# Kernel tuning notes

Measured on AMD Instinct MI355X. Metric: run time of the kernel, lower is better.

Reference implementation:

```python
import jax, jax.numpy as jnp
import numpy as np

LAYERS = 3       # opt.layer
B = 4096         # batch of sessions
MAX_LEN = 200    # padded session length
N_ITEMS = 100000 # item vocab (index 0 is PAD after zero-row concat)
E = 112          # emb_size (SessConv default)
EPS = 1e-12      # F.normalize eps


def setup_inputs() -> dict:
    key = jax.random.key(0)
    k0, k1, k2, k3, k4 = jax.random.split(key, 5)
    item_embedding = jax.random.normal(k0, (N_ITEMS, E), dtype=jnp.float32) * 0.1
    # Session-session adjacency A and diagonal inverse-degree D (so D @ A is row-normalized)
    A = jax.random.uniform(k1, (B, B), dtype=jnp.float32)
    D = jnp.diag(1.0 / A.sum(axis=1))
    # Padded session item indices; 0 == PAD row (zeros prepended to the table)
    session_item = jax.random.randint(k2, (B, MAX_LEN), 0, N_ITEMS + 1, dtype=jnp.int64)
    session_len = jax.random.randint(k3, (B, 1), 1, MAX_LEN + 1).astype(jnp.float32)
    # layers x Linear(E, E, bias=False) weights, torch layout [out, in]
    Ws = jax.random.normal(k4, (LAYERS, E, E), dtype=jnp.float32) * (1.0 / np.sqrt(E))
    return {"item_embedding": item_embedding, "D": D, "A": A,
            "session_len": session_len, "Ws": Ws, "session_item": session_item}


def reference(item_embedding, D, A, session_len, Ws, session_item):
    # Prepend zero row so index 0 gathers zeros (padding)
    emb = jnp.concatenate([jnp.zeros((1, E), item_embedding.dtype), item_embedding], axis=0)
    # Fused ragged gather + mean-pool (replaces per-session index_select + cpu/numpy roundtrip)
    seq_h = emb[session_item]                       # [B, MAX_LEN, E]
    session_emb = seq_h.sum(axis=1) / session_len   # [B, E]
    DA = D @ A                                      # [B, B]
    acc = session_emb                               # layer-0 term of the final average
    for i in range(LAYERS):
        session_emb = session_emb @ Ws[i].T         # Linear(E,E,bias=False)
        session_emb = DA @ session_emb              # session graph propagation
        nrm = jnp.linalg.norm(session_emb, axis=-1, keepdims=True)
        acc = acc + session_emb / jnp.maximum(nrm, EPS)  # appended term is L2-normalized
        # NOTE: next layer consumes the UN-normalized session_emb (as in the torch code)
    return acc / (LAYERS + 1)
```

## Files before the change

kernel.cpp:

```cpp
#include <hip/hip_runtime.h>
#include <hip/hip_bf16.h>

#define BSZ 4096
#define MAXLEN 200
#define EDIM 112
#define NKC 16

typedef __attribute__((ext_vector_type(8))) short bf16x8;
typedef __attribute__((ext_vector_type(4))) float f32x4;

static __device__ __forceinline__ short f2bf(float f) {
    unsigned u = __float_as_uint(f);
    unsigned r = (u + 0x7fffu + ((u >> 16) & 1u)) >> 16;
    return (short)r;
}
static __device__ __forceinline__ float bf2f(short s) {
    return __uint_as_float(((unsigned)(unsigned short)s) << 16);
}
static __device__ __forceinline__ bf16x8 cvt8(float4 a, float4 b) {
    bf16x8 r;
    r[0] = f2bf(a.x); r[1] = f2bf(a.y); r[2] = f2bf(a.z); r[3] = f2bf(a.w);
    r[4] = f2bf(b.x); r[5] = f2bf(b.y); r[6] = f2bf(b.z); r[7] = f2bf(b.w);
    return r;
}
static __device__ __forceinline__ unsigned pack2(float a, float b) {
    return ((unsigned)f2bf(a) & 0xffffu) | ((unsigned)f2bf(b) << 16);
}

__global__ __launch_bounds__(256) void f32_to_bf16(const float* __restrict__ src,
                                                   unsigned short* __restrict__ dst,
                                                   int ngroups, int zgroups) {
    int g = blockIdx.x * 256 + threadIdx.x;
    if (g >= ngroups) return;
    bf16x8 o;
    if (g < zgroups) {
        #pragma unroll
        for (int i = 0; i < 8; ++i) o[i] = 0;
    } else {
        const float* p = src + (size_t)(g - zgroups) * 8;
        float4 a = *(const float4*)p;
        float4 b = *(const float4*)(p + 4);
        o = cvt8(a, b);
    }
    *(bf16x8*)(dst + (size_t)g * 8) = o;
}

__global__ __launch_bounds__(256) void gather_pool_bf(const unsigned short* __restrict__ Ebf,
                                                      const int* __restrict__ items,
                                                      const float* __restrict__ slen,
                                                      float* __restrict__ S,
                                                      float* __restrict__ acc) {
    __shared__ float part[16][14][8];
    int wave = threadIdx.x >> 6;
    int lane = threadIdx.x & 63;
    int b = blockIdx.x;
    int rg = lane / 14;
    int c  = lane % 14;
    const int* it = items + (size_t)b * MAXLEN + wave * 50;
    float a[8];
    #pragma unroll
    for (int e = 0; e < 8; ++e) a[e] = 0.f;
    if (lane < 56) {
        #pragma unroll
        for (int t = 0; t < 13; ++t) {
            int j = t * 4 + rg;
            int idx = 0;
            if (j < 50) idx = it[j];
            bf16x8 v = *(const bf16x8*)(Ebf + (size_t)idx * EDIM + c * 8);
            #pragma unroll
            for (int e = 0; e < 8; ++e) a[e] += bf2f(v[e]);
        }
        #pragma unroll
        for (int e = 0; e < 8; ++e) part[wave * 4 + rg][c][e] = a[e];
    }
    __syncthreads();
    int tid = threadIdx.x;
    if (tid < EDIM) {
        int cc = tid >> 3, ee = tid & 7;
        float s = 0.f;
        #pragma unroll
        for (int g = 0; g < 16; ++g) s += part[g][cc][ee];
        s /= slen[b];
        S[(size_t)b * EDIM + tid]   = s;
        acc[(size_t)b * EDIM + tid] = s;
    }
}

static __device__ __forceinline__ bf16x8 ldcvt(const float* p, bool valid) {
    if (valid) {
        float4 a = *(const float4*)p;
        float4 b = *(const float4*)(p + 4);
        return cvt8(a, b);
    }
    bf16x8 z;
    #pragma unroll
    for (int i = 0; i < 8; ++i) z[i] = 0;
    return z;
}

template <int MODE>
__global__ __launch_bounds__(64, 4) void fused_mid(const float* __restrict__ Sin,
                                                   const float* __restrict__ Yp,
                                                   const float* __restrict__ Dm,
                                                   float* __restrict__ accb,
                                                   const float* __restrict__ W,
                                                   unsigned short* __restrict__ Bsw) {
    __shared__ unsigned short Ylds[16][136];
    int lane = threadIdx.x;
    int gw = blockIdx.x;
    int j0 = gw * 16;
    int nrow = lane & 15;
    int quad = lane >> 4;
    int ses = j0 + nrow;

    float4 v[7];
    if (MODE == 0) {
        const float4* p = (const float4*)(Sin + (size_t)ses * EDIM + quad * 28);
        #pragma unroll
        for (int i = 0; i < 7; ++i) v[i] = p[i];
    } else {
        #pragma unroll
        for (int i = 0; i < 7; ++i) v[i] = make_float4(0.f, 0.f, 0.f, 0.f);
        #pragma unroll 4
        for (int pp = 0; pp < NKC; ++pp) {
            const float4* p = (const float4*)(Yp + (size_t)pp * BSZ * EDIM
                                              + (size_t)ses * EDIM + quad * 28);
            #pragma unroll
            for (int i = 0; i < 7; ++i) {
                float4 t = p[i];
                v[i].x += t.x; v[i].y += t.y; v[i].z += t.z; v[i].w += t.w;
            }
        }
        float d = Dm[(size_t)ses * (BSZ + 1)];
        float ss = 0.f;
        #pragma unroll
        for (int i = 0; i < 7; ++i) {
            v[i].x *= d; v[i].y *= d; v[i].z *= d; v[i].w *= d;
            ss += v[i].x * v[i].x + v[i].y * v[i].y + v[i].z * v[i].z + v[i].w * v[i].w;
        }
        ss += __shfl_xor(ss, 16, 64);
        ss += __shfl_xor(ss, 32, 64);
        float rinv = 1.f / fmaxf(sqrtf(ss), 1e-12f);
        float4* pa = (float4*)(accb + (size_t)ses * EDIM + quad * 28);
        #pragma unroll
        for (int i = 0; i < 7; ++i) {
            float4 a = pa[i];
            a.x += v[i].x * rinv; a.y += v[i].y * rinv;
            a.z += v[i].z * rinv; a.w += v[i].w * rinv;
            pa[i] = a;
        }
    }

    #pragma unroll
    for (int i = 0; i < 7; ++i) {
        uint2 pk;
        pk.x = pack2(v[i].x, v[i].y);
        pk.y = pack2(v[i].z, v[i].w);
        *(uint2*)&Ylds[nrow][quad * 28 + i * 4] = pk;
    }
    *(uint2*)&Ylds[nrow][112 + quad * 4] = make_uint2(0u, 0u);
    __syncthreads();

    bf16x8 aF[4];
    #pragma unroll
    for (int k32 = 0; k32 < 4; ++k32)
        aF[k32] = *(bf16x8*)&Ylds[nrow][k32 * 32 + quad * 8];

    f32x4 acc[7];
    #pragma unroll
    for (int t = 0; t < 7; ++t) acc[t] = (f32x4){0.f, 0.f, 0.f, 0.f};
    #pragma unroll
    for (int t = 0; t < 7; ++t) {
        const float* wr = W + (size_t)(16 * t + nrow) * EDIM;
        #pragma unroll
        for (int k32 = 0; k32 < 4; ++k32) {
            bf16x8 bF = ldcvt(wr + k32 * 32 + quad * 8, (k32 < 3) || (quad < 2));
            acc[t] = __builtin_amdgcn_mfma_f32_16x16x32_bf16(aF[k32], bF, acc[t], 0, 0, 0);
        }
    }

    int k32f = j0 >> 5;
    int qp = ((j0 >> 4) & 1) * 2 + (quad >> 1);
    int e0 = (quad & 1) * 4;
    #pragma unroll
    for (int t = 0; t < 7; ++t) {
        uint2 pk;
        pk.x = pack2(acc[t][0], acc[t][1]);
        pk.y = pack2(acc[t][2], acc[t][3]);
        *(uint2*)(Bsw + ((size_t)(k32f * 7 + t) * 64 + qp * 16 + nrow) * 8 + e0) = pk;
    }
}

template <int AMODE>
__global__ __launch_bounds__(64, 4) void big_gemm(const float* __restrict__ Af,
                                                  unsigned short* __restrict__ Asw,
                                                  const unsigned short* __restrict__ Bsw,
                                                  float* __restrict__ Yp) {
    int lane = threadIdx.x;
    int mt2 = blockIdx.x & 127;
    int kc = blockIdx.x >> 7;
    int nrow = lane & 15;
    int quad = lane >> 4;

    f32x4 acc[2][7];
    #pragma unroll
    for (int s = 0; s < 2; ++s)
        #pragma unroll
        for (int t = 0; t < 7; ++t) acc[s][t] = (f32x4){0.f, 0.f, 0.f, 0.f};

    for (int ks = 0; ks < 8; ++ks) {
        int k32 = kc * 8 + ks;
        bf16x8 aF[2];
        #pragma unroll
        for (int sub = 0; sub < 2; ++sub) {
            int mtile = mt2 * 2 + sub;
            size_t afrag = ((size_t)(mtile * 128 + k32) * 64 + lane) * 8;
            if (AMODE == 0) {
                const float* p = Af + (size_t)(mtile * 16 + nrow) * 4096 + k32 * 32 + quad * 8;
                float4 a0 = *(const float4*)p;
                float4 a1 = *(const float4*)(p + 4);
                aF[sub] = cvt8(a0, a1);
                *(bf16x8*)(Asw + afrag) = aF[sub];
            } else {
                aF[sub] = *(const bf16x8*)(Asw + afrag);
            }
        }
        const unsigned short* bb = Bsw + ((size_t)k32 * 7 * 64 + lane) * 8;
        #pragma unroll
        for (int t = 0; t < 7; ++t) {
            bf16x8 bF = *(const bf16x8*)(bb + (size_t)t * 512);
            acc[0][t] = __builtin_amdgcn_mfma_f32_16x16x32_bf16(aF[0], bF, acc[0][t], 0, 0, 0);
            acc[1][t] = __builtin_amdgcn_mfma_f32_16x16x32_bf16(aF[1], bF, acc[1][t], 0, 0, 0);
        }
    }

    float* dst = Yp + (size_t)kc * BSZ * EDIM + (size_t)mt2 * 32 * EDIM;
    #pragma unroll
    for (int sub = 0; sub < 2; ++sub)
        #pragma unroll
        for (int t = 0; t < 7; ++t)
            #pragma unroll
            for (int r = 0; r < 4; ++r)
                dst[(size_t)(sub * 16 + quad * 4 + r) * EDIM + 16 * t + nrow] = acc[sub][t][r];
}

__global__ __launch_bounds__(256) void final_epilogue(const float* __restrict__ Yp,
                                                      const float* __restrict__ Dm,
                                                      const float* __restrict__ accb,
                                                      float* __restrict__ out) {
    int wave = threadIdx.x >> 6;
    int lane = threadIdx.x & 63;
    int b = blockIdx.x * 4 + wave;

    float2 v = make_float2(0.f, 0.f);
    size_t o2 = (size_t)b * 56 + lane;
    if (lane < 56) {
        #pragma unroll 4
        for (int p = 0; p < NKC; ++p) {
            float2 t = ((const float2*)(Yp + (size_t)p * BSZ * EDIM))[o2];
            v.x += t.x;
            v.y += t.y;
        }
    }
    float d = Dm[(size_t)b * (BSZ + 1)];
    v.x *= d; v.y *= d;
    float ss = v.x * v.x + v.y * v.y;
    #pragma unroll
    for (int off = 32; off; off >>= 1) ss += __shfl_xor(ss, off, 64);
    float nrm = fmaxf(sqrtf(ss), 1e-12f);
    if (lane < 56) {
        float2 a = ((const float2*)accb)[o2];
        ((float2*)out)[o2] = make_float2((a.x + v.x / nrm) * 0.25f,
                                         (a.y + v.y / nrm) * 0.25f);
    }
}

extern "C" void kernel_launch(void* const* d_in, const int* in_sizes, int n_in,
                              void* d_out, int out_size, void* d_ws, size_t ws_size,
                              hipStream_t stream) {
    (void)in_sizes; (void)n_in; (void)out_size; (void)ws_size;
    const float* emb   = (const float*)d_in[0];
    const float* Dm    = (const float*)d_in[1];
    const float* A     = (const float*)d_in[2];
    const float* slen  = (const float*)d_in[3];
    const float* Ws    = (const float*)d_in[4];
    const int*   items = (const int*)d_in[5];
    float* out = (float*)d_out;

    char* w = (char*)d_ws;
    float* Sa   = (float*)w;
    float* accb = Sa + BSZ * EDIM;
    float* Yp   = accb + BSZ * EDIM;
    unsigned short* Bsw = (unsigned short*)(Yp + (size_t)NKC * BSZ * EDIM);
    unsigned short* Ebf = Bsw + 128 * 7 * 64 * 8;
    unsigned short* Asw = Ebf + 100001 * EDIM;

    f32_to_bf16<<<5470, 256, 0, stream>>>(emb, Ebf, 1400014, 14);
    gather_pool_bf<<<BSZ, 256, 0, stream>>>(Ebf, items, slen, Sa, accb);
    fused_mid<0><<<256, 64, 0, stream>>>(Sa, nullptr, nullptr, nullptr, Ws, Bsw);
    big_gemm<0><<<2048, 64, 0, stream>>>(A, Asw, Bsw, Yp);
    fused_mid<1><<<256, 64, 0, stream>>>(nullptr, Yp, Dm, accb,
                                         Ws + (size_t)EDIM * EDIM, Bsw);
    big_gemm<1><<<2048, 64, 0, stream>>>(nullptr, Asw, Bsw, Yp);
    fused_mid<1><<<256, 64, 0, stream>>>(nullptr, Yp, Dm, accb,
                                         Ws + (size_t)2 * EDIM * EDIM, Bsw);
    big_gemm<1><<<2048, 64, 0, stream>>>(nullptr, Asw, Bsw, Yp);
    final_epilogue<<<BSZ / 4, 256, 0, stream>>>(Yp, Dm, accb, out);
}
```

Measured before the change: 288.9 us.

## Fuse split-K reduction, normalize and next-layer linear into big GEMM blocks

Each big GEMM block now covers one 16-row M tile with 8 waves splitting K across the whole 4096 dimension. It reduces the partial sums in LDS instead of writing 16 split-K partials to global memory. The D scaling, L2 normalization, accumulator update and the next layer's 112x112 linear are done in the same kernel, with ping-pong B buffers, which removes the separate mid and final epilogue kernels and the Yp round-trip. The K loop is also software-pipelined with register prefetch. The trade-off is only 256 blocks of 512 threads and heavy LDS use, which may underfill the GPU.

```diff
diff --git a/kernel.cpp b/kernel.cpp
--- a/kernel.cpp
+++ b/kernel.cpp
@@ -4,7 +4,7 @@
 #define BSZ 4096
 #define MAXLEN 200
 #define EDIM 112
-#define NKC 16
+#define NW 8
 
 typedef __attribute__((ext_vector_type(8))) short bf16x8;
 typedef __attribute__((ext_vector_type(4))) float f32x4;
@@ -88,7 +88,7 @@
 
 static __device__ __forceinline__ bf16x8 ldcvt(const float* p, bool valid) {
     if (valid) {
-        float4 a = *(const float4*)p;
+        float4 a = *(const float4*)(p);
         float4 b = *(const float4*)(p + 4);
         return cvt8(a, b);
     }
@@ -98,13 +98,9 @@
     return z;
 }
 
-template <int MODE>
-__global__ __launch_bounds__(64, 4) void fused_mid(const float* __restrict__ Sin,
-                                                   const float* __restrict__ Yp,
-                                                   const float* __restrict__ Dm,
-                                                   float* __restrict__ accb,
-                                                   const float* __restrict__ W,
-                                                   unsigned short* __restrict__ Bsw) {
+__global__ __launch_bounds__(64, 4) void fused_mid0(const float* __restrict__ Sin,
+                                                    const float* __restrict__ W,
+                                                    unsigned short* __restrict__ Bsw) {
     __shared__ unsigned short Ylds[16][136];
     int lane = threadIdx.x;
     int gw = blockIdx.x;
@@ -114,42 +110,9 @@
     int ses = j0 + nrow;
 
     float4 v[7];
-    if (MODE == 0) {
-        const float4* p = (const float4*)(Sin + (size_t)ses * EDIM + quad * 28);
-        #pragma unroll
-        for (int i = 0; i < 7; ++i) v[i] = p[i];
-    } else {
-        #pragma unroll
-        for (int i = 0; i < 7; ++i) v[i] = make_float4(0.f, 0.f, 0.f, 0.f);
-        #pragma unroll 4
-        for (int pp = 0; pp < NKC; ++pp) {
-            const float4* p = (const float4*)(Yp + (size_t)pp * BSZ * EDIM
-                                              + (size_t)ses * EDIM + quad * 28);
-            #pragma unroll
-            for (int i = 0; i < 7; ++i) {
-                float4 t = p[i];
-                v[i].x += t.x; v[i].y += t.y; v[i].z += t.z; v[i].w += t.w;
-            }
-        }
-        float d = Dm[(size_t)ses * (BSZ + 1)];
-        float ss = 0.f;
-        #pragma unroll
-        for (int i = 0; i < 7; ++i) {
-            v[i].x *= d; v[i].y *= d; v[i].z *= d; v[i].w *= d;
-            ss += v[i].x * v[i].x + v[i].y * v[i].y + v[i].z * v[i].z + v[i].w * v[i].w;
-        }
-        ss += __shfl_xor(ss, 16, 64);
-        ss += __shfl_xor(ss, 32, 64);
-        float rinv = 1.f / fmaxf(sqrtf(ss), 1e-12f);
-        float4* pa = (float4*)(accb + (size_t)ses * EDIM + quad * 28);
-        #pragma unroll
-        for (int i = 0; i < 7; ++i) {
-            float4 a = pa[i];
-            a.x += v[i].x * rinv; a.y += v[i].y * rinv;
-            a.z += v[i].z * rinv; a.w += v[i].w * rinv;
-            pa[i] = a;
-        }
-    }
+    const float4* p = (const float4*)(Sin + (size_t)ses * EDIM + quad * 28);
+    #pragma unroll
+    for (int i = 0; i < 7; ++i) v[i] = p[i];
 
     #pragma unroll
     for (int i = 0; i < 7; ++i) {
@@ -191,87 +154,145 @@
     }
 }
 
-template <int AMODE>
-__global__ __launch_bounds__(64, 4) void big_gemm(const float* __restrict__ Af,
-                                                  unsigned short* __restrict__ Asw,
-                                                  const unsigned short* __restrict__ Bsw,
-                                                  float* __restrict__ Yp) {
-    int lane = threadIdx.x;
-    int mt2 = blockIdx.x & 127;
-    int kc = blockIdx.x >> 7;
+template <int AMODE, int LAST>
+__global__ __launch_bounds__(512, 2) void bg_fused(const float* __restrict__ Af,
+                                                   unsigned short* __restrict__ Asw,
+                                                   const unsigned short* __restrict__ Bsw,
+                                                   const float* __restrict__ Dm,
+                                                   float* __restrict__ accb,
+                                                   const float* __restrict__ W,
+                                                   unsigned short* __restrict__ BswOut,
+                                                   float* __restrict__ out) {
+    __shared__ float part[NW][16][116];
+    __shared__ unsigned short Ylds[16][136];
+    int tid = threadIdx.x;
+    int w = tid >> 6;
+    int lane = tid & 63;
     int nrow = lane & 15;
     int quad = lane >> 4;
-
-    f32x4 acc[2][7];
-    #pragma unroll
-    for (int s = 0; s < 2; ++s)
-        #pragma unroll
-        for (int t = 0; t < 7; ++t) acc[s][t] = (f32x4){0.f, 0.f, 0.f, 0.f};
-
-    for (int ks = 0; ks < 8; ++ks) {
-        int k32 = kc * 8 + ks;
-        bf16x8 aF[2];
-        #pragma unroll
-        for (int sub = 0; sub < 2; ++sub) {
-            int mtile = mt2 * 2 + sub;
-            size_t afrag = ((size_t)(mtile * 128 + k32) * 64 + lane) * 8;
-            if (AMODE == 0) {
-                const float* p = Af + (size_t)(mtile * 16 + nrow) * 4096 + k32 * 32 + quad * 8;
-                float4 a0 = *(const float4*)p;
-                float4 a1 = *(const float4*)(p + 4);
-                aF[sub] = cvt8(a0, a1);
-                *(bf16x8*)(Asw + afrag) = aF[sub];
-            } else {
-                aF[sub] = *(const bf16x8*)(Asw + afrag);
+    int mtile = blockIdx.x;
+
+    f32x4 acc[7];
+    #pragma unroll
+    for (int t = 0; t < 7; ++t) acc[t] = (f32x4){0.f, 0.f, 0.f, 0.f};
+
+    auto LOADA = [&](int k32) -> bf16x8 {
+        size_t afrag = ((size_t)(mtile * 128 + k32) * 64 + lane) * 8;
+        if (AMODE == 0) {
+            const float* p = Af + (size_t)(mtile * 16 + nrow) * 4096 + k32 * 32 + quad * 8;
+            float4 a0 = *(const float4*)p;
+            float4 a1 = *(const float4*)(p + 4);
+            bf16x8 r = cvt8(a0, a1);
+            *(bf16x8*)(Asw + afrag) = r;
+            return r;
+        } else {
+            return *(const bf16x8*)(Asw + afrag);
+        }
+    };
+
+    int k32 = w * 16;
+    bf16x8 aF = LOADA(k32);
+    bf16x8 bF[7];
+    {
+        const unsigned short* bb = Bsw + ((size_t)k32 * 7 * 64 + lane) * 8;
+        #pragma unroll
+        for (int t = 0; t < 7; ++t) bF[t] = *(const bf16x8*)(bb + (size_t)t * 512);
+    }
+    #pragma unroll 1
+    for (int ks = 0; ks < 15; ++ks) {
+        bf16x8 aN = LOADA(k32 + 1);
+        bf16x8 bN[7];
+        const unsigned short* bb = Bsw + ((size_t)(k32 + 1) * 7 * 64 + lane) * 8;
+        #pragma unroll
+        for (int t = 0; t < 7; ++t) bN[t] = *(const bf16x8*)(bb + (size_t)t * 512);
+        #pragma unroll
+        for (int t = 0; t < 7; ++t)
+            acc[t] = __builtin_amdgcn_mfma_f32_16x16x32_bf16(aF, bF[t], acc[t], 0, 0, 0);
+        aF = aN;
+        #pragma unroll
+        for (int t = 0; t < 7; ++t) bF[t] = bN[t];
+        ++k32;
+    }
+    #pragma unroll
+    for (int t = 0; t < 7; ++t)
+        acc[t] = __builtin_amdgcn_mfma_f32_16x16x32_bf16(aF, bF[t], acc[t], 0, 0, 0);
+
+    #pragma unroll
+    for (int t = 0; t < 7; ++t)
+        #pragma unroll
+        for (int r = 0; r < 4; ++r)
+            part[w][quad * 4 + r][16 * t + nrow] = acc[t][r];
+    __syncthreads();
+
+    int half = lane >> 5;
+    int cg = lane & 31;
+    int row = 2 * w + half;
+    int grow = mtile * 16 + row;
+    int col = cg * 4;
+    float4 v = make_float4(0.f, 0.f, 0.f, 0.f);
+    if (cg < 28) {
+        #pragma unroll
+        for (int p = 0; p < NW; ++p) {
+            float4 t = *(const float4*)&part[p][row][col];
+            v.x += t.x; v.y += t.y; v.z += t.z; v.w += t.w;
+        }
+    }
+    float d = Dm[(size_t)grow * (BSZ + 1)];
+    v.x *= d; v.y *= d; v.z *= d; v.w *= d;
+    float ss = v.x * v.x + v.y * v.y + v.z * v.z + v.w * v.w;
+    ss += __shfl_xor(ss, 1, 64);
+    ss += __shfl_xor(ss, 2, 64);
+    ss += __shfl_xor(ss, 4, 64);
+    ss += __shfl_xor(ss, 8, 64);
+    ss += __shfl_xor(ss, 16, 64);
+    float rinv = 1.f / fmaxf(sqrtf(ss), 1e-12f);
+    if (cg < 28) {
+        if (LAST) {
+            float4 a = *(const float4*)(accb + (size_t)grow * EDIM + col);
+            float4 o;
+            o.x = (a.x + v.x * rinv) * 0.25f;
+            o.y = (a.y + v.y * rinv) * 0.25f;
+            o.z = (a.z + v.z * rinv) * 0.25f;
+            o.w = (a.w + v.w * rinv) * 0.25f;
+            *(float4*)(out + (size_t)grow * EDIM + col) = o;
+        } else {
+            float4* pa = (float4*)(accb + (size_t)grow * EDIM + col);
+            float4 a = *pa;
+            a.x += v.x * rinv; a.y += v.y * rinv;
+            a.z += v.z * rinv; a.w += v.w * rinv;
+            *pa = a;
+        }
+    }
+
+    if (!LAST) {
+        uint2 pk;
+        pk.x = pack2(v.x, v.y);
+        pk.y = pack2(v.z, v.w);
+        *(uint2*)&Ylds[row][col] = pk;
+        __syncthreads();
+
+        if (w < 7) {
+            int t = w;
+            bf16x8 aF2[4];
+            #pragma unroll
+            for (int k = 0; k < 4; ++k)
+                aF2[k] = *(bf16x8*)&Ylds[nrow][k * 32 + quad * 8];
+            f32x4 c = (f32x4){0.f, 0.f, 0.f, 0.f};
+            const float* wr = W + (size_t)(16 * t + nrow) * EDIM;
+            #pragma unroll
+            for (int k = 0; k < 4; ++k) {
+                bf16x8 bW = ldcvt(wr + k * 32 + quad * 8, (k < 3) || (quad < 2));
+                c = __builtin_amdgcn_mfma_f32_16x16x32_bf16(aF2[k], bW, c, 0, 0, 0);
             }
-        }
-        const unsigned short* bb = Bsw + ((size_t)k32 * 7 * 64 + lane) * 8;
-        #pragma unroll
-        for (int t = 0; t < 7; ++t) {
-            bf16x8 bF = *(const bf16x8*)(bb + (size_t)t * 512);
-            acc[0][t] = __builtin_amdgcn_mfma_f32_16x16x32_bf16(aF[0], bF, acc[0][t], 0, 0, 0);
-            acc[1][t] = __builtin_amdgcn_mfma_f32_16x16x32_bf16(aF[1], bF, acc[1][t], 0, 0, 0);
-        }
-    }
-
-    float* dst = Yp + (size_t)kc * BSZ * EDIM + (size_t)mt2 * 32 * EDIM;
-    #pragma unroll
-    for (int sub = 0; sub < 2; ++sub)
-        #pragma unroll
-        for (int t = 0; t < 7; ++t)
-            #pragma unroll
-            for (int r = 0; r < 4; ++r)
-                dst[(size_t)(sub * 16 + quad * 4 + r) * EDIM + 16 * t + nrow] = acc[sub][t][r];
-}
-
-__global__ __launch_bounds__(256) void final_epilogue(const float* __restrict__ Yp,
-                                                      const float* __restrict__ Dm,
-                                                      const float* __restrict__ accb,
-                                                      float* __restrict__ out) {
-    int wave = threadIdx.x >> 6;
-    int lane = threadIdx.x & 63;
-    int b = blockIdx.x * 4 + wave;
-
-    float2 v = make_float2(0.f, 0.f);
-    size_t o2 = (size_t)b * 56 + lane;
-    if (lane < 56) {
-        #pragma unroll 4
-        for (int p = 0; p < NKC; ++p) {
-            float2 t = ((const float2*)(Yp + (size_t)p * BSZ * EDIM))[o2];
-            v.x += t.x;
-            v.y += t.y;
-        }
-    }
-    float d = Dm[(size_t)b * (BSZ + 1)];
-    v.x *= d; v.y *= d;
-    float ss = v.x * v.x + v.y * v.y;
-    #pragma unroll
-    for (int off = 32; off; off >>= 1) ss += __shfl_xor(ss, off, 64);
-    float nrm = fmaxf(sqrtf(ss), 1e-12f);
-    if (lane < 56) {
-        float2 a = ((const float2*)accb)[o2];
-        ((float2*)out)[o2] = make_float2((a.x + v.x / nrm) * 0.25f,
-                                         (a.y + v.y / nrm) * 0.25f);
+            int j0 = mtile * 16;
+            int k32f = j0 >> 5;
+            int qp = ((j0 >> 4) & 1) * 2 + (quad >> 1);
+            int e0 = (quad & 1) * 4;
+            uint2 ck;
+            ck.x = pack2(c[0], c[1]);
+            ck.y = pack2(c[2], c[3]);
+            *(uint2*)(BswOut + ((size_t)(k32f * 7 + t) * 64 + qp * 16 + nrow) * 8 + e0) = ck;
+        }
     }
 }
 
@@ -290,20 +311,18 @@
     char* w = (char*)d_ws;
     float* Sa   = (float*)w;
     float* accb = Sa + BSZ * EDIM;
-    float* Yp   = accb + BSZ * EDIM;
-    unsigned short* Bsw = (unsigned short*)(Yp + (size_t)NKC * BSZ * EDIM);
-    unsigned short* Ebf = Bsw + 128 * 7 * 64 * 8;
-    unsigned short* Asw = Ebf + 100001 * EDIM;
+    unsigned short* Bsw0 = (unsigned short*)(accb + BSZ * EDIM);
+    unsigned short* Bsw1 = Bsw0 + (size_t)128 * 7 * 64 * 8;
+    unsigned short* Ebf  = Bsw1 + (size_t)128 * 7 * 64 * 8;
+    unsigned short* Asw  = Ebf + (size_t)100001 * EDIM;
 
     f32_to_bf16<<<5470, 256, 0, stream>>>(emb, Ebf, 1400014, 14);
     gather_pool_bf<<<BSZ, 256, 0, stream>>>(Ebf, items, slen, Sa, accb);
-    fused_mid<0><<<256, 64, 0, stream>>>(Sa, nullptr, nullptr, nullptr, Ws, Bsw);
-    big_gemm<0><<<2048, 64, 0, stream>>>(A, Asw, Bsw, Yp);
-    fused_mid<1><<<256, 64, 0, stream>>>(nullptr, Yp, Dm, accb,
-                                         Ws + (size_t)EDIM * EDIM, Bsw);
-    big_gemm<1><<<2048, 64, 0, stream>>>(nullptr, Asw, Bsw, Yp);
-    fused_mid<1><<<256, 64, 0, stream>>>(nullptr, Yp, Dm, accb,
-                                         Ws + (size_t)2 * EDIM * EDIM, Bsw);
-    big_gemm<1><<<2048, 64, 0, stream>>>(nullptr, Asw, Bsw, Yp);
-    final_epilogue<<<BSZ / 4, 256, 0, stream>>>(Yp, Dm, accb, out);
-}
+    fused_mid0<<<256, 64, 0, stream>>>(Sa, Ws, Bsw0);
+    bg_fused<0, 0><<<256, 512, 0, stream>>>(A, Asw, Bsw0, Dm, accb,
+                                            Ws + (size_t)EDIM * EDIM, Bsw1, nullptr);
+    bg_fused<1, 0><<<256, 512, 0, stream>>>(nullptr, Asw, Bsw1, Dm, accb,
+                                            Ws + (size_t)2 * EDIM * EDIM, Bsw0, nullptr);
+    bg_fused<1, 1><<<256, 512, 0, stream>>>(nullptr, Asw, Bsw0, Dm, accb,
+                                            nullptr, nullptr, out);
+}
```

Result: faster. 253.7 us (-12.2%).

## Restructure big GEMM into 8-wave blocks with LDS split-K reduction

Applied to the files above, without the earlier changes.

The big DA-propagation GEMM changes from 64-thread blocks over 32 rows and 16 K-chunks to 512-thread blocks over 16 rows. Each of the 8 waves handles 4 K-steps, loads for the next step are issued before the current MFMAs, and partial results are summed in LDS with atomics. Only 4 partial slices go to global memory instead of 16, which shrinks Yp traffic and the reduction work in the mid and final epilogues. Bsw is double-buffered across layers. In exchange each wave gets much less reuse of the B fragment per A load, and LDS atomics are added.

```diff
diff --git a/kernel.cpp b/kernel.cpp
--- a/kernel.cpp
+++ b/kernel.cpp
@@ -4,7 +4,7 @@
 #define BSZ 4096
 #define MAXLEN 200
 #define EDIM 112
-#define NKC 16
+#define NPL 4
 
 typedef __attribute__((ext_vector_type(8))) short bf16x8;
 typedef __attribute__((ext_vector_type(4))) float f32x4;
@@ -88,7 +88,7 @@
 
 static __device__ __forceinline__ bf16x8 ldcvt(const float* p, bool valid) {
     if (valid) {
-        float4 a = *(const float4*)p;
+        float4 a = *(const float4*)(p);
         float4 b = *(const float4*)(p + 4);
         return cvt8(a, b);
     }
@@ -98,13 +98,9 @@
     return z;
 }
 
-template <int MODE>
-__global__ __launch_bounds__(64, 4) void fused_mid(const float* __restrict__ Sin,
-                                                   const float* __restrict__ Yp,
-                                                   const float* __restrict__ Dm,
-                                                   float* __restrict__ accb,
-                                                   const float* __restrict__ W,
-                                                   unsigned short* __restrict__ Bsw) {
+__global__ __launch_bounds__(64, 4) void fused_mid0(const float* __restrict__ Sin,
+                                                    const float* __restrict__ W,
+                                                    unsigned short* __restrict__ Bsw) {
     __shared__ unsigned short Ylds[16][136];
     int lane = threadIdx.x;
     int gw = blockIdx.x;
@@ -114,42 +110,9 @@
     int ses = j0 + nrow;
 
     float4 v[7];
-    if (MODE == 0) {
-        const float4* p = (const float4*)(Sin + (size_t)ses * EDIM + quad * 28);
-        #pragma unroll
-        for (int i = 0; i < 7; ++i) v[i] = p[i];
-    } else {
-        #pragma unroll
-        for (int i = 0; i < 7; ++i) v[i] = make_float4(0.f, 0.f, 0.f, 0.f);
-        #pragma unroll 4
-        for (int pp = 0; pp < NKC; ++pp) {
-            const float4* p = (const float4*)(Yp + (size_t)pp * BSZ * EDIM
-                                              + (size_t)ses * EDIM + quad * 28);
-            #pragma unroll
-            for (int i = 0; i < 7; ++i) {
-                float4 t = p[i];
-                v[i].x += t.x; v[i].y += t.y; v[i].z += t.z; v[i].w += t.w;
-            }
-        }
-        float d = Dm[(size_t)ses * (BSZ + 1)];
-        float ss = 0.f;
-        #pragma unroll
-        for (int i = 0; i < 7; ++i) {
-            v[i].x *= d; v[i].y *= d; v[i].z *= d; v[i].w *= d;
-            ss += v[i].x * v[i].x + v[i].y * v[i].y + v[i].z * v[i].z + v[i].w * v[i].w;
-        }
-        ss += __shfl_xor(ss, 16, 64);
-        ss += __shfl_xor(ss, 32, 64);
-        float rinv = 1.f / fmaxf(sqrtf(ss), 1e-12f);
-        float4* pa = (float4*)(accb + (size_t)ses * EDIM + quad * 28);
-        #pragma unroll
-        for (int i = 0; i < 7; ++i) {
-            float4 a = pa[i];
-            a.x += v[i].x * rinv; a.y += v[i].y * rinv;
-            a.z += v[i].z * rinv; a.w += v[i].w * rinv;
-            pa[i] = a;
-        }
-    }
+    const float4* p = (const float4*)(Sin + (size_t)ses * EDIM + quad * 28);
+    #pragma unroll
+    for (int i = 0; i < 7; ++i) v[i] = p[i];
 
     #pragma unroll
     for (int i = 0; i < 7; ++i) {
@@ -192,56 +155,166 @@
 }
 
 template <int AMODE>
-__global__ __launch_bounds__(64, 4) void big_gemm(const float* __restrict__ Af,
-                                                  unsigned short* __restrict__ Asw,
-                                                  const unsigned short* __restrict__ Bsw,
-                                                  float* __restrict__ Yp) {
-    int lane = threadIdx.x;
-    int mt2 = blockIdx.x & 127;
-    int kc = blockIdx.x >> 7;
+__global__ __launch_bounds__(512, 4) void bg_gemm4(const float* __restrict__ Af,
+                                                   unsigned short* __restrict__ Asw,
+                                                   const unsigned short* __restrict__ Bsw,
+                                                   float* __restrict__ Yp) {
+    __shared__ float part[16][120];
+    int tid = threadIdx.x;
+    int w = tid >> 6;
+    int lane = tid & 63;
     int nrow = lane & 15;
     int quad = lane >> 4;
-
-    f32x4 acc[2][7];
-    #pragma unroll
-    for (int s = 0; s < 2; ++s)
-        #pragma unroll
-        for (int t = 0; t < 7; ++t) acc[s][t] = (f32x4){0.f, 0.f, 0.f, 0.f};
-
-    for (int ks = 0; ks < 8; ++ks) {
-        int k32 = kc * 8 + ks;
-        bf16x8 aF[2];
-        #pragma unroll
-        for (int sub = 0; sub < 2; ++sub) {
-            int mtile = mt2 * 2 + sub;
-            size_t afrag = ((size_t)(mtile * 128 + k32) * 64 + lane) * 8;
-            if (AMODE == 0) {
-                const float* p = Af + (size_t)(mtile * 16 + nrow) * 4096 + k32 * 32 + quad * 8;
-                float4 a0 = *(const float4*)p;
-                float4 a1 = *(const float4*)(p + 4);
-                aF[sub] = cvt8(a0, a1);
-                *(bf16x8*)(Asw + afrag) = aF[sub];
-            } else {
-                aF[sub] = *(const bf16x8*)(Asw + afrag);
-            }
-        }
+    int mtile = blockIdx.x & 255;
+    int kq = blockIdx.x >> 8;
+
+    if (tid < 480) ((float4*)part)[tid] = make_float4(0.f, 0.f, 0.f, 0.f);
+    __syncthreads();
+
+    f32x4 acc[7];
+    #pragma unroll
+    for (int t = 0; t < 7; ++t) acc[t] = (f32x4){0.f, 0.f, 0.f, 0.f};
+
+    auto LOADA = [&](int k32) -> bf16x8 {
+        size_t afrag = ((size_t)(mtile * 128 + k32) * 64 + lane) * 8;
+        if (AMODE == 0) {
+            const float* p = Af + (size_t)(mtile * 16 + nrow) * 4096 + k32 * 32 + quad * 8;
+            float4 a0 = *(const float4*)p;
+            float4 a1 = *(const float4*)(p + 4);
+            bf16x8 r = cvt8(a0, a1);
+            *(bf16x8*)(Asw + afrag) = r;
+            return r;
+        } else {
+            return *(const bf16x8*)(Asw + afrag);
+        }
+    };
+
+    int k32 = kq * 32 + w * 4;
+    bf16x8 aF = LOADA(k32);
+    bf16x8 bF[7];
+    {
         const unsigned short* bb = Bsw + ((size_t)k32 * 7 * 64 + lane) * 8;
         #pragma unroll
-        for (int t = 0; t < 7; ++t) {
-            bf16x8 bF = *(const bf16x8*)(bb + (size_t)t * 512);
-            acc[0][t] = __builtin_amdgcn_mfma_f32_16x16x32_bf16(aF[0], bF, acc[0][t], 0, 0, 0);
-            acc[1][t] = __builtin_amdgcn_mfma_f32_16x16x32_bf16(aF[1], bF, acc[1][t], 0, 0, 0);
-        }
-    }
-
-    float* dst = Yp + (size_t)kc * BSZ * EDIM + (size_t)mt2 * 32 * EDIM;
-    #pragma unroll
-    for (int sub = 0; sub < 2; ++sub)
+        for (int t = 0; t < 7; ++t) bF[t] = *(const bf16x8*)(bb + (size_t)t * 512);
+    }
+    #pragma unroll
+    for (int ks = 0; ks < 3; ++ks) {
+        bf16x8 aN = LOADA(k32 + 1);
+        bf16x8 bN[7];
+        const unsigned short* bb = Bsw + ((size_t)(k32 + 1) * 7 * 64 + lane) * 8;
+        #pragma unroll
+        for (int t = 0; t < 7; ++t) bN[t] = *(const bf16x8*)(bb + (size_t)t * 512);
         #pragma unroll
         for (int t = 0; t < 7; ++t)
-            #pragma unroll
-            for (int r = 0; r < 4; ++r)
-                dst[(size_t)(sub * 16 + quad * 4 + r) * EDIM + 16 * t + nrow] = acc[sub][t][r];
+            acc[t] = __builtin_amdgcn_mfma_f32_16x16x32_bf16(aF, bF[t], acc[t], 0, 0, 0);
+        aF = aN;
+        #pragma unroll
+        for (int t = 0; t < 7; ++t) bF[t] = bN[t];
+        ++k32;
+    }
+    #pragma unroll
+    for (int t = 0; t < 7; ++t)
+        acc[t] = __builtin_amdgcn_mfma_f32_16x16x32_bf16(aF, bF[t], acc[t], 0, 0, 0);
+
+    #pragma unroll
+    for (int t = 0; t < 7; ++t)
+        #pragma unroll
+        for (int r = 0; r < 4; ++r)
+            atomicAdd(&part[quad * 4 + r][16 * t + nrow], acc[t][r]);
+    __syncthreads();
+
+    if (tid < 448) {
+        int row16 = tid / 28;
+        int col = (tid - row16 * 28) * 4;
+        float4 v = *(const float4*)&part[row16][col];
+        *(float4*)(Yp + (size_t)kq * BSZ * EDIM
+                   + (size_t)(mtile * 16 + row16) * EDIM + col) = v;
+    }
+}
+
+__global__ __launch_bounds__(64, 4) void epi_mid(const float* __restrict__ Yp,
+                                                 const float* __restrict__ Dm,
+                                                 float* __restrict__ accb,
+                                                 const float* __restrict__ W,
+                                                 unsigned short* __restrict__ Bsw) {
+    __shared__ unsigned short Ylds[16][136];
+    int lane = threadIdx.x;
+    int gw = blockIdx.x;
+    int j0 = gw * 16;
+    int nrow = lane & 15;
+    int quad = lane >> 4;
+    int ses = j0 + nrow;
+
+    float4 v[7];
+    #pragma unroll
+    for (int i = 0; i < 7; ++i) v[i] = make_float4(0.f, 0.f, 0.f, 0.f);
+    #pragma unroll
+    for (int pp = 0; pp < NPL; ++pp) {
+        const float4* p = (const float4*)(Yp + (size_t)pp * BSZ * EDIM
+                                          + (size_t)ses * EDIM + quad * 28);
+        #pragma unroll
+        for (int i = 0; i < 7; ++i) {
+            float4 t = p[i];
+            v[i].x += t.x; v[i].y += t.y; v[i].z += t.z; v[i].w += t.w;
+        }
+    }
+    float d = Dm[(size_t)ses * (BSZ + 1)];
+    float ss = 0.f;
+    #pragma unroll
+    for (int i = 0; i < 7; ++i) {
+        v[i].x *= d; v[i].y *= d; v[i].z *= d; v[i].w *= d;
+        ss += v[i].x * v[i].x + v[i].y * v[i].y + v[i].z * v[i].z + v[i].w * v[i].w;
+    }
+    ss += __shfl_xor(ss, 16, 64);
+    ss += __shfl_xor(ss, 32, 64);
+    float rinv = 1.f / fmaxf(sqrtf(ss), 1e-12f);
+    float4* pa = (float4*)(accb + (size_t)ses * EDIM + quad * 28);
+    #pragma unroll
+    for (int i = 0; i < 7; ++i) {
+        float4 a = pa[i];
+        a.x += v[i].x * rinv; a.y += v[i].y * rinv;
+        a.z += v[i].z * rinv; a.w += v[i].w * rinv;
+        pa[i] = a;
+    }
+
+    #pragma unroll
+    for (int i = 0; i < 7; ++i) {
+        uint2 pk;
+        pk.x = pack2(v[i].x, v[i].y);
+        pk.y = pack2(v[i].z, v[i].w);
+        *(uint2*)&Ylds[nrow][quad * 28 + i * 4] = pk;
+    }
+    *(uint2*)&Ylds[nrow][112 + quad * 4] = make_uint2(0u, 0u);
+    __syncthreads();
+
+    bf16x8 aF[4];
+    #pragma unroll
+    for (int k32 = 0; k32 < 4; ++k32)
+        aF[k32] = *(bf16x8*)&Ylds[nrow][k32 * 32 + quad * 8];
+
+    f32x4 acc[7];
+    #pragma unroll
+    for (int t = 0; t < 7; ++t) acc[t] = (f32x4){0.f, 0.f, 0.f, 0.f};
+    #pragma unroll
+    for (int t = 0; t < 7; ++t) {
+        const float* wr = W + (size_t)(16 * t + nrow) * EDIM;
+        #pragma unroll
+        for (int k32 = 0; k32 < 4; ++k32) {
+            bf16x8 bF = ldcvt(wr + k32 * 32 + quad * 8, (k32 < 3) || (quad < 2));
+            acc[t] = __builtin_amdgcn_mfma_f32_16x16x32_bf16(aF[k32], bF, acc[t], 0, 0, 0);
+        }
+    }
+
+    int k32f = j0 >> 5;
+    int qp = ((j0 >> 4) & 1) * 2 + (quad >> 1);
+    int e0 = (quad & 1) * 4;
+    #pragma unroll
+    for (int t = 0; t < 7; ++t) {
+        uint2 pk;
+        pk.x = pack2(acc[t][0], acc[t][1]);
+        pk.y = pack2(acc[t][2], acc[t][3]);
+        *(uint2*)(Bsw + ((size_t)(k32f * 7 + t) * 64 + qp * 16 + nrow) * 8 + e0) = pk;
+    }
 }
 
 __global__ __launch_bounds__(256) void final_epilogue(const float* __restrict__ Yp,
@@ -255,8 +328,8 @@
     float2 v = make_float2(0.f, 0.f);
     size_t o2 = (size_t)b * 56 + lane;
     if (lane < 56) {
-        #pragma unroll 4
-        for (int p = 0; p < NKC; ++p) {
+        #pragma unroll
+        for (int p = 0; p < NPL; ++p) {
             float2 t = ((const float2*)(Yp + (size_t)p * BSZ * EDIM))[o2];
             v.x += t.x;
             v.y += t.y;
@@ -291,19 +364,18 @@
     float* Sa   = (float*)w;
     float* accb = Sa + BSZ * EDIM;
     float* Yp   = accb + BSZ * EDIM;
-    unsigned short* Bsw = (unsigned short*)(Yp + (size_t)NKC * BSZ * EDIM);
-    unsigned short* Ebf = Bsw + 128 * 7 * 64 * 8;
-    unsigned short* Asw = Ebf + 100001 * EDIM;
+    unsigned short* Bsw0 = (unsigned short*)(Yp + (size_t)NPL * BSZ * EDIM);
+    unsigned short* Bsw1 = Bsw0 + (size_t)128 * 7 * 64 * 8;
+    unsigned short* Ebf  = Bsw1 + (size_t)128 * 7 * 64 * 8;
+    unsigned short* Asw  = Ebf + (size_t)100001 * EDIM;
 
     f32_to_bf16<<<5470, 256, 0, stream>>>(emb, Ebf, 1400014, 14);
     gather_pool_bf<<<BSZ, 256, 0, stream>>>(Ebf, items, slen, Sa, accb);
-    fused_mid<0><<<256, 64, 0, stream>>>(Sa, nullptr, nullptr, nullptr, Ws, Bsw);
-    big_gemm<0><<<2048, 64, 0, stream>>>(A, Asw, Bsw, Yp);
-    fused_mid<1><<<256, 64, 0, stream>>>(nullptr, Yp, Dm, accb,
-                                         Ws + (size_t)EDIM * EDIM, Bsw);
-    big_gemm<1><<<2048, 64, 0, stream>>>(nullptr, Asw, Bsw, Yp);
-    fused_mid<1><<<256, 64, 0, stream>>>(nullptr, Yp, Dm, accb,
-                                         Ws + (size_t)2 * EDIM * EDIM, Bsw);
-    big_gemm<1><<<2048, 64, 0, stream>>>(nullptr, Asw, Bsw, Yp);
+    fused_mid0<<<256, 64, 0, stream>>>(Sa, Ws, Bsw0);
+    bg_gemm4<0><<<1024, 512, 0, stream>>>(A, Asw, Bsw0, Yp);
+    epi_mid<<<256, 64, 0, stream>>>(Yp, Dm, accb, Ws + (size_t)EDIM * EDIM, Bsw1);
+    bg_gemm4<1><<<1024, 512, 0, stream>>>(nullptr, Asw, Bsw1, Yp);
+    epi_mid<<<256, 64, 0, stream>>>(Yp, Dm, accb, Ws + (size_t)2 * EDIM * EDIM, Bsw0);
+    bg_gemm4<1><<<1024, 512, 0, stream>>>(nullptr, Asw, Bsw0, Yp);
     final_epilogue<<<BSZ / 4, 256, 0, stream>>>(Yp, Dm, accb, out);
 }
```

After: 470.6 us. 1.63x slower.
